# Kernel optimization log

Measured on AMD Instinct MI355X. Metric: run time of the kernel, lower is better.

The kernel has to match this reference:

```python
import jax, jax.numpy as jnp
import numpy as np

D = 1024      # embedding_size
H = 16        # num_heads
HD = D // H   # head_size
EPS = 1e-5


def setup_inputs() -> dict:
    key = jax.random.key(0)
    ks = jax.random.split(key, 12)
    s_in = 1.0 / np.sqrt(D)
    s_hid = 1.0 / np.sqrt(4 * D)
    return {
        "x": jax.random.normal(ks[0], (2, 2048, D), dtype=jnp.float32),
        # per-head projections, no bias: [H, D, HD]
        "Wq": jax.random.normal(ks[1], (H, D, HD), dtype=jnp.float32) * s_in,
        "Wk": jax.random.normal(ks[2], (H, D, HD), dtype=jnp.float32) * s_in,
        "Wv": jax.random.normal(ks[3], (H, D, HD), dtype=jnp.float32) * s_in,
        "Wo": jax.random.normal(ks[4], (D, D), dtype=jnp.float32) * s_in,
        "bo": jnp.zeros((D,), dtype=jnp.float32),
        "W1": jax.random.normal(ks[5], (D, 4 * D), dtype=jnp.float32) * s_in,
        "b1": jnp.zeros((4 * D,), dtype=jnp.float32),
        "W2": jax.random.normal(ks[6], (4 * D, D), dtype=jnp.float32) * s_hid,
        "b2": jnp.zeros((D,), dtype=jnp.float32),
        "g1": jnp.ones((D,), dtype=jnp.float32),
        "be1": jnp.zeros((D,), dtype=jnp.float32),
        "g2": jnp.ones((D,), dtype=jnp.float32),
        "be2": jnp.zeros((D,), dtype=jnp.float32),
    }


def _layernorm(x, g, b):
    mu = jnp.mean(x, axis=-1, keepdims=True)
    var = jnp.mean(jnp.square(x - mu), axis=-1, keepdims=True)
    return (x - mu) * jax.lax.rsqrt(var + EPS) * g + b


def _block(x, Wq, Wk, Wv, Wo, bo, W1, b1, W2, b2, g1, be1, g2, be2):
    B, T, _ = x.shape
    h = _layernorm(x, g1, be1)
    # per-head projections: [B, H, T, HD]
    q = jnp.einsum('btd,hde->bhte', h, Wq)
    k = jnp.einsum('btd,hde->bhte', h, Wk)
    v = jnp.einsum('btd,hde->bhte', h, Wv)
    # NOTE: original scales by embedding_size**-0.5 (x.shape[-1]), not head_size
    scores = jnp.einsum('bhte,bhse->bhts', q, k) * (D ** -0.5)
    mask = jnp.tril(jnp.ones((T, T), dtype=bool))
    scores = jnp.where(mask, scores, -jnp.inf)
    attn = jax.nn.softmax(scores, axis=-1)           # dropout = identity (eval)
    out = jnp.einsum('bhts,bhse->bhte', attn, v)      # [B, H, T, HD]
    out = out.transpose(0, 2, 1, 3).reshape(B, T, D)  # concat heads
    x = x + (out @ Wo + bo)
    h2 = _layernorm(x, g2, be2)
    ffn = jax.nn.relu(h2 @ W1 + b1) @ W2 + b2
    return x + ffn


def reference(x, Wq, Wk, Wv, Wo, bo, W1, b1, W2, b2, g1, be1, g2, be2):
    return _block(x, Wq, Wk, Wv, Wo, bo, W1, b1, W2, b2, g1, be1, g2, be2)
```

## Files before the change

### kernel.cpp

```cpp
#include <hip/hip_runtime.h>
#include <stdint.h>

typedef unsigned short u16;
typedef __attribute__((ext_vector_type(8))) __bf16 bf16x8;
typedef __attribute__((ext_vector_type(4))) float f32x4;

#define D_EMB 1024
#define NHEAD 16
#define HDIM 64
#define TSEQ 2048
#define NTOK 4096
#define NEG_BIG -1.0e30f

#define GLD16(lp, gp) __builtin_amdgcn_global_load_lds( \
    (const __attribute__((address_space(1))) unsigned int*)(gp), \
    (__attribute__((address_space(3))) unsigned int*)(lp), 16, 0, 0)

__device__ __forceinline__ float bf2f(u16 u) {
    union { unsigned int i; float f; } c; c.i = ((unsigned int)u) << 16; return c.f;
}
__device__ __forceinline__ u16 f2bf(float f) {
    union { float f; unsigned int i; } c; c.f = f;
    unsigned int r = (c.i + 0x7FFFu + ((c.i >> 16) & 1u)) >> 16;
    return (u16)r;
}
__device__ __forceinline__ void cp16(u16* dst, const u16* src) {
    *reinterpret_cast<uint4*>(dst) = *reinterpret_cast<const uint4*>(src);
}
__device__ __forceinline__ float load_in(const u16* p, size_t idx, int f32) {
    return f32 ? reinterpret_cast<const float*>(p)[idx] : bf2f(p[idx]);
}
__device__ __forceinline__ size_t tidx(int row, int col, int KB) {
    int c = (col & 7) | ((((col >> 3) ^ row) & 3) << 3);
    return ((size_t)((row >> 7) * KB + (col >> 5)) * 128 + (row & 127)) * 32 + c;
}

__global__ void detect_kernel(const u16* __restrict__ x, u16* __restrict__ fl) {
    if (threadIdx.x == 0) {
        int f = 0;
        for (int i = 0; i < 128; ++i) {
            float v = fabsf(bf2f(x[i]));
            if (!(v <= 1.0e3f)) f = 1;
        }
        fl[0] = (u16)f;
    }
}

__global__ __launch_bounds__(256) void transpose_tiled_kernel(
        const u16* __restrict__ X, u16* __restrict__ Xt, int KB,
        const u16* __restrict__ fl) {
    __shared__ __align__(16) u16 Ts[64 * 72];
    int f32 = fl[0];
    int bi = blockIdx.y, bj = blockIdx.x;
    int NS = gridDim.x * 64;
    int t = threadIdx.x;
    for (int p = 0; p < 2; ++p) {
        int idx = p * 256 + t;
        int row = idx >> 3, col8 = (idx & 7) * 8;
        size_t src = (size_t)(bi * 64 + row) * NS + bj * 64 + col8;
        if (f32) {
            for (int jj = 0; jj < 8; ++jj)
                Ts[row * 72 + col8 + jj] = f2bf(reinterpret_cast<const float*>(X)[src + jj]);
        } else {
            cp16(&Ts[row * 72 + col8], &X[src]);
        }
    }
    __syncthreads();
    for (int p = 0; p < 2; ++p) {
        int idx = p * 256 + t;
        int row = idx >> 3, col8 = (idx & 7) * 8;
        union { u16 u[8]; uint4 v; } tmp;
        for (int jj = 0; jj < 8; ++jj) tmp.u[jj] = Ts[(col8 + jj) * 72 + row];
        int n = bj * 64 + row, k0 = bi * 64 + col8;
        *reinterpret_cast<uint4*>(&Xt[tidx(n, k0, KB)]) = tmp.v;
    }
}

__global__ __launch_bounds__(256) void pack_qkv_kernel(
        const u16* __restrict__ Wq, const u16* __restrict__ Wk,
        const u16* __restrict__ Wv, u16* __restrict__ Wt,
        const u16* __restrict__ fl) {
    int f32 = fl[0];
    int idx = blockIdx.x * 256 + threadIdx.x;
    int e = idx & 63, d = (idx >> 6) & 1023, hh = (idx >> 16) & 15, sel = idx >> 20;
    const u16* W = (sel == 0) ? Wq : ((sel == 1) ? Wk : Wv);
    size_t src = (size_t)hh * (D_EMB * HDIM) + (size_t)d * HDIM + e;
    float v = f32 ? reinterpret_cast<const float*>(W)[src] : bf2f(W[src]);
    int n = sel * 1024 + hh * 64 + e;
    Wt[tidx(n, d, 32)] = f2bf(v);
}

__global__ __launch_bounds__(256) void ln_kernel(
        const u16* __restrict__ X, const u16* __restrict__ g,
        const u16* __restrict__ be, u16* __restrict__ Ht,
        const u16* __restrict__ fl) {
    int f32 = fl[0];
    int row = blockIdx.x;
    int t = threadIdx.x;
    float v[4];
    float s = 0.f, sq = 0.f;
    for (int i = 0; i < 4; ++i) {
        v[i] = load_in(X, (size_t)row * D_EMB + t + i * 256, f32);
        s += v[i]; sq += v[i] * v[i];
    }
    for (int m = 32; m; m >>= 1) { s += __shfl_down(s, m); sq += __shfl_down(sq, m); }
    __shared__ float red[8];
    int wid = t >> 6, lane = t & 63;
    if (lane == 0) { red[wid] = s; red[wid + 4] = sq; }
    __syncthreads();
    if (t == 0) {
        float S = red[0] + red[1] + red[2] + red[3];
        float SQ = red[4] + red[5] + red[6] + red[7];
        float mean = S * (1.f / 1024.f);
        float var = SQ * (1.f / 1024.f) - mean * mean;
        red[0] = mean; red[1] = rsqrtf(var + 1e-5f);
    }
    __syncthreads();
    float mean = red[0], rstd = red[1];
    for (int i = 0; i < 4; ++i) {
        int c = t + i * 256;
        float hv = (v[i] - mean) * rstd * load_in(g, c, f32) + load_in(be, c, f32);
        Ht[tidx(row, c, 32)] = f2bf(hv);
    }
}

template<int TAG, int TN>
__global__ __launch_bounds__(256) void gemm_t(
        const u16* __restrict__ At, const u16* __restrict__ Bt, u16* __restrict__ C,
        u16* __restrict__ C2,
        const u16* __restrict__ bias, const u16* __restrict__ res,
        int N, int K, int flags, int row_off,
        const u16* __restrict__ fl) {
    constexpr int NF = (TN == 128) ? 4 : 2;
    __shared__ __align__(16) u16 As2[2][4096];
    __shared__ __align__(16) u16 Bs2[2][TN * 32];
    int f32 = fl[0];
    int t = threadIdx.x;
    int gx = gridDim.x, gy = gridDim.y;
    int id = blockIdx.y * gx + blockIdx.x;
    int total = gx * gy;
    int xcd = id & 7, seq = id >> 3, P = total >> 3;
    int tpb = (P >= 32) ? 32 : 16;
    int th  = (P >= 32) ? 8 : 4;
    int tile = xcd * (P / tpb) + seq / tpb;
    int within = seq % tpb;
    int tiles_x = gx >> 2;
    int bx = (tile % tiles_x) * 4 + (within & 3);
    int by = (tile / tiles_x) * th + (within >> 2);
    int n0 = bx * TN, m0 = by * 128;
    int w = t >> 6, lane = t & 63, quad = lane >> 4, l16 = lane & 15;
    int wm = (TN == 128) ? (w >> 1) * 64 : (w & 1) * 64;
    int wn = (TN == 128) ? (w & 1) * 64  : (w >> 1) * 32;
    int KB = K >> 5;
    int kb0 = (seq * (KB >> 5)) & (KB - 1);
    const u16* Ab = At + (size_t)(m0 >> 7) * KB * 4096 + w * 512 + lane * 8;
    const u16* Bb = Bt + (size_t)(n0 >> 7) * KB * 4096
                       + ((TN == 64) ? (n0 & 64) * 32 : 0) + w * 512 + lane * 8;

    auto stage = [&](int buf, int kb) {
        const u16* ga = Ab + (size_t)kb * 4096;
        const u16* gb = Bb + (size_t)kb * 4096;
        u16* la = &As2[buf][w * 512];
        u16* lb = &Bs2[buf][w * 512];
        GLD16(la, ga);
        GLD16(la + 2048, ga + 2048);
        GLD16(lb, gb);
        if constexpr (TN == 128) { GLD16(lb + 2048, gb + 2048); }
    };

    const f32x4 fz = {0.f, 0.f, 0.f, 0.f};
    f32x4 acc[4][NF];
    for (int mt = 0; mt < 4; ++mt)
        for (int nt = 0; nt < NF; ++nt) acc[mt][nt] = fz;

    stage(0, kb0);
    __syncthreads();
    int kb = kb0;
    for (int it = 0; it < KB; ++it) {
        int cur = it & 1;
        int kn = (kb + 1 == KB) ? 0 : kb + 1;
        if (it + 1 < KB) stage(cur ^ 1, kn);
        bf16x8 af[4], bfr[NF];
        for (int mt = 0; mt < 4; ++mt) {
            int r = wm + mt * 16 + l16;
            af[mt] = *reinterpret_cast<const bf16x8*>(
                &As2[cur][r * 32 + (((quad ^ r) & 3) << 3)]);
        }
        for (int nt = 0; nt < NF; ++nt) {
            int r = wn + nt * 16 + l16;
            bfr[nt] = *reinterpret_cast<const bf16x8*>(
                &Bs2[cur][r * 32 + (((quad ^ r) & 3) << 3)]);
        }
        for (int mt = 0; mt < 4; ++mt)
            for (int nt = 0; nt < NF; ++nt)
                acc[mt][nt] = __builtin_amdgcn_mfma_f32_16x16x32_bf16(af[mt], bfr[nt], acc[mt][nt], 0, 0, 0);
        __syncthreads();
        kb = kn;
    }

    int relu_f = flags & 1, out_ext = flags & 2, c_tiled = flags & 4, qkvsp = flags & 8;
    if (qkvsp) {
        for (int mt = 0; mt < 4; ++mt)
            for (int nt = 0; nt < NF; ++nt) {
                int gc = n0 + wn + nt * 16 + l16;
                int grb = m0 + wm + mt * 16 + quad * 4;
                if (gc < 2048) {
                    for (int r = 0; r < 4; ++r)
                        C[(size_t)(grb + r) * 2048 + gc] = f2bf(acc[mt][nt][r]);
                } else {
                    int hh = (gc - 2048) >> 6, d = gc & 63;
                    int bb = grb >> 11, s = grb & 2047;
                    union { u16 u[4]; uint2 v; } pk;
                    for (int r = 0; r < 4; ++r) pk.u[r] = f2bf(acc[mt][nt][r]);
                    *reinterpret_cast<uint2*>(
                        &C2[(((size_t)bb * 16 + hh) * 64 + d) * 2048 + s]) = pk.v;
                }
            }
        return;
    }
    for (int mt = 0; mt < 4; ++mt)
        for (int nt = 0; nt < NF; ++nt)
            for (int r = 0; r < 4; ++r) {
                int gr = m0 + wm + mt * 16 + quad * 4 + r;
                int gc = n0 + wn + nt * 16 + l16;
                float v = acc[mt][nt][r];
                if (bias) v += load_in(bias, gc, f32);
                if (relu_f) v = v > 0.f ? v : 0.f;
                size_t oidx = (size_t)(row_off + gr) * N + gc;
                if (res) v += load_in(res, oidx, f32);
                if (c_tiled)      C[tidx(gr, gc, N >> 5)] = f2bf(v);
                else if (out_ext && f32) reinterpret_cast<float*>(C)[oidx] = v;
                else              C[oidx] = f2bf(v);
            }
}

template<int TAG, int KBL, int TN>
__global__ __launch_bounds__(256) void gemm_sk_t(
        const u16* __restrict__ At, const u16* __restrict__ Bt,
        float* __restrict__ Pp, int N, int K) {
    constexpr int NF = (TN == 128) ? 4 : 2;
    __shared__ __align__(16) u16 As2[2][4096];
    __shared__ __align__(16) u16 Bs2[2][TN * 32];
    int t = threadIdx.x;
    int gx = gridDim.x, gy = gridDim.y;
    int id = blockIdx.y * gx + blockIdx.x;
    int total = gx * gy;
    int xcd = id & 7, seq = id >> 3, P = total >> 3;
    int tpb = (P >= 32) ? 32 : 16;
    int th  = (P >= 32) ? 8 : 4;
    int tile = xcd * (P / tpb) + seq / tpb;
    int within = seq % tpb;
    int tiles_x = gx >> 2;
    int bx = (tile % tiles_x) * 4 + (within & 3);
    int by = (tile / tiles_x) * th + (within >> 2);
    int n0 = bx * TN, m0 = by * 128;
    int w = t >> 6, lane = t & 63, quad = lane >> 4, l16 = lane & 15;
    int wm = (TN == 128) ? (w >> 1) * 64 : (w & 1) * 64;
    int wn = (TN == 128) ? (w & 1) * 64  : (w >> 1) * 32;
    int KB = K >> 5;
    int kstart = blockIdx.z * KBL;
    int rel0 = seq & (KBL - 1);
    const u16* Ab = At + (size_t)(m0 >> 7) * KB * 4096 + w * 512 + lane * 8;
    const u16* Bb = Bt + (size_t)(n0 >> 7) * KB * 4096
                       + ((TN == 64) ? (n0 & 64) * 32 : 0) + w * 512 + lane * 8;

    auto stage = [&](int buf, int kb) {
        const u16* ga = Ab + (size_t)kb * 4096;
        const u16* gb = Bb + (size_t)kb * 4096;
        u16* la = &As2[buf][w * 512];
        u16* lb = &Bs2[buf][w * 512];
        GLD16(la, ga);
        GLD16(la + 2048, ga + 2048);
        GLD16(lb, gb);
        if constexpr (TN == 128) { GLD16(lb + 2048, gb + 2048); }
    };

    const f32x4 fz = {0.f, 0.f, 0.f, 0.f};
    f32x4 acc[4][NF];
    for (int mt = 0; mt < 4; ++mt)
        for (int nt = 0; nt < NF; ++nt) acc[mt][nt] = fz;

    stage(0, kstart + rel0);
    __syncthreads();
    for (int it = 0; it < KBL; ++it) {
        int cur = it & 1;
        if (it + 1 < KBL)
            stage(cur ^ 1, kstart + ((rel0 + it + 1) & (KBL - 1)));
        bf16x8 af[4], bfr[NF];
        for (int mt = 0; mt < 4; ++mt) {
            int r = wm + mt * 16 + l16;
            af[mt] = *reinterpret_cast<const bf16x8*>(
                &As2[cur][r * 32 + (((quad ^ r) & 3) << 3)]);
        }
        for (int nt = 0; nt < NF; ++nt) {
            int r = wn + nt * 16 + l16;
            bfr[nt] = *reinterpret_cast<const bf16x8*>(
                &Bs2[cur][r * 32 + (((quad ^ r) & 3) << 3)]);
        }
        for (int mt = 0; mt < 4; ++mt)
            for (int nt = 0; nt < NF; ++nt)
                acc[mt][nt] = __builtin_amdgcn_mfma_f32_16x16x32_bf16(af[mt], bfr[nt], acc[mt][nt], 0, 0, 0);
        __syncthreads();
    }

    for (int mt = 0; mt < 4; ++mt)
        for (int nt = 0; nt < NF; ++nt)
            for (int r = 0; r < 4; ++r) {
                int gr = m0 + wm + mt * 16 + quad * 4 + r;
                int gc = n0 + wn + nt * 16 + l16;
                atomicAdd(&Pp[(size_t)gr * N + gc], acc[mt][nt][r]);
            }
}

__global__ __launch_bounds__(256) void zero_f32_kernel(float* __restrict__ p) {
    const f32x4 fz = {0.f, 0.f, 0.f, 0.f};
    reinterpret_cast<f32x4*>(p)[(size_t)blockIdx.x * 256 + threadIdx.x] = fz;
}

__global__ __launch_bounds__(256) void ffn_fin_kernel(
        const float* __restrict__ Pp, const u16* __restrict__ b2,
        u16* __restrict__ out, int row_off, const u16* __restrict__ fl) {
    int f32 = fl[0];
    size_t i = ((size_t)blockIdx.x * 256 + threadIdx.x) * 4;
    int col = (int)(i & 1023);
    f32x4 pv = *reinterpret_cast<const f32x4*>(Pp + i);
    size_t o = (size_t)row_off * 1024 + i;
    if (f32) {
        float* of = reinterpret_cast<float*>(out);
        f32x4 ov = *reinterpret_cast<f32x4*>(of + o);
        for (int j = 0; j < 4; ++j)
            ov[j] += pv[j] + load_in(b2, col + j, 1);
        *reinterpret_cast<f32x4*>(of + o) = ov;
    } else {
        for (int j = 0; j < 4; ++j) {
            float v = bf2f(out[o + j]) + pv[j] + bf2f(b2[col + j]);
            out[o + j] = f2bf(v);
        }
    }
}

__global__ __launch_bounds__(256) void oproj_fin_kernel(
        const float* __restrict__ Pp, const u16* __restrict__ bo,
        const u16* __restrict__ x, u16* __restrict__ out,
        const u16* __restrict__ fl) {
    int f32 = fl[0];
    size_t i = ((size_t)blockIdx.x * 256 + threadIdx.x) * 4;
    int col = (int)(i & 1023);
    f32x4 pv = *reinterpret_cast<const f32x4*>(Pp + i);
    if (f32) {
        const float* xf = reinterpret_cast<const float*>(x);
        float* of = reinterpret_cast<float*>(out);
        f32x4 ov;
        for (int j = 0; j < 4; ++j)
            ov[j] = xf[i + j] + pv[j] + load_in(bo, col + j, 1);
        *reinterpret_cast<f32x4*>(of + i) = ov;
    } else {
        for (int j = 0; j < 4; ++j) {
            float v = bf2f(x[i + j]) + pv[j] + bf2f(bo[col + j]);
            out[i + j] = f2bf(v);
        }
    }
}

__global__ __launch_bounds__(128) void flash_kernel(
        const u16* __restrict__ qk, const u16* __restrict__ vt,
        u16* __restrict__ attn_t) {
    __shared__ __align__(16) u16 Ps[32 * 72];
    int t = threadIdx.x;
    int px = blockIdx.x & 15, rh = blockIdx.x >> 4;
    int b = blockIdx.y >> 4, h = blockIdx.y & 15;
    int wid = t >> 6, lane = t & 63, quad = lane >> 4, l16 = lane & 15;
    int g = rh * 2 + wid;
    const size_t seq_base = (size_t)b * TSEQ;
    const u16* vplane = vt + (size_t)(b * 16 + h) * 64 * 2048;

    for (int half = 0; half < 2; ++half) {
        int tq = half ? px : (31 - px);

        bf16x8 aq[2];
        for (int kit = 0; kit < 2; ++kit)
            aq[kit] = *reinterpret_cast<const bf16x8*>(
                &qk[(seq_base + tq * 64 + g * 16 + l16) * 2048 + h * 64 + kit * 32 + quad * 8]);

        const f32x4 fz = {0.f, 0.f, 0.f, 0.f};
        float m_run[4], l_run[4];
        f32x4 o[4];
        for (int r = 0; r < 4; ++r) { m_run[r] = NEG_BIG; l_run[r] = 0.f; }
        for (int nt = 0; nt < 4; ++nt) o[nt] = fz;

        for (int j = 0; j <= tq; ++j) {
            f32x4 sa[4];
            for (int nt = 0; nt < 4; ++nt) sa[nt] = fz;
            for (int kit = 0; kit < 2; ++kit) {
                for (int nt = 0; nt < 4; ++nt) {
                    bf16x8 bk = *reinterpret_cast<const bf16x8*>(
                        &qk[(seq_base + j * 64 + nt * 16 + l16) * 2048 + 1024 + h * 64 + kit * 32 + quad * 8]);
                    sa[nt] = __builtin_amdgcn_mfma_f32_16x16x32_bf16(aq[kit], bk, sa[nt], 0, 0, 0);
                }
            }

            float p_val[4][4];
            int qbase = tq * 64 + g * 16 + quad * 4;
            int sbase = j * 64 + l16;
            for (int r = 0; r < 4; ++r) {
                float sv[4];
                float mx = NEG_BIG;
                for (int nt = 0; nt < 4; ++nt) {
                    float xv = sa[nt][r] * 0.03125f;
                    if (sbase + nt * 16 > qbase + r) xv = NEG_BIG;
                    sv[nt] = xv;
                    mx = fmaxf(mx, xv);
                }
                for (int m = 1; m < 16; m <<= 1) mx = fmaxf(mx, __shfl_xor(mx, m));
                float mnew = fmaxf(m_run[r], mx);
                float alpha = __expf(m_run[r] - mnew);
                m_run[r] = mnew;
                float rs = 0.f;
                for (int nt = 0; nt < 4; ++nt) {
                    float pv = __expf(sv[nt] - mnew);
                    p_val[nt][r] = pv;
                    rs += pv;
                }
                for (int m = 1; m < 16; m <<= 1) rs += __shfl_xor(rs, m);
                l_run[r] = l_run[r] * alpha + rs;
                for (int nt = 0; nt < 4; ++nt) o[nt][r] *= alpha;
            }

            for (int nt = 0; nt < 4; ++nt)
                for (int r = 0; r < 4; ++r)
                    Ps[(wid * 16 + quad * 4 + r) * 72 + nt * 16 + l16] = f2bf(p_val[nt][r]);

            for (int kit = 0; kit < 2; ++kit) {
                bf16x8 ap = *reinterpret_cast<const bf16x8*>(
                    &Ps[(wid * 16 + l16) * 72 + kit * 32 + quad * 8]);
                for (int nt = 0; nt < 4; ++nt) {
                    bf16x8 bv = *reinterpret_cast<const bf16x8*>(
                        &vplane[(size_t)(nt * 16 + l16) * 2048 + j * 64 + kit * 32 + quad * 8]);
                    o[nt] = __builtin_amdgcn_mfma_f32_16x16x32_bf16(ap, bv, o[nt], 0, 0, 0);
                }
            }
        }

        for (int nt = 0; nt < 4; ++nt)
            for (int r = 0; r < 4; ++r) {
                int trow = (int)seq_base + tq * 64 + g * 16 + quad * 4 + r;
                int col = h * 64 + nt * 16 + l16;
                attn_t[tidx(trow, col, 32)] = f2bf(o[nt][r] / l_run[r]);
            }
    }
}

extern "C" void kernel_launch(void* const* d_in, const int* in_sizes, int n_in,
                              void* d_out, int out_size, void* d_ws, size_t ws_size,
                              hipStream_t stream) {
    const u16* x   = (const u16*)d_in[0];
    const u16* Wq  = (const u16*)d_in[1];
    const u16* Wk  = (const u16*)d_in[2];
    const u16* Wv  = (const u16*)d_in[3];
    const u16* Wo  = (const u16*)d_in[4];
    const u16* bo  = (const u16*)d_in[5];
    const u16* W1  = (const u16*)d_in[6];
    const u16* b1  = (const u16*)d_in[7];
    const u16* W2  = (const u16*)d_in[8];
    const u16* b2  = (const u16*)d_in[9];
    const u16* g1  = (const u16*)d_in[10];
    const u16* be1 = (const u16*)d_in[11];
    const u16* g2  = (const u16*)d_in[12];
    const u16* be2 = (const u16*)d_in[13];
    u16* out = (u16*)d_out;

    const size_t M1 = (size_t)1 << 20;
    u16* ws    = (u16*)d_ws;
    u16* qk    = ws;
    u16* vt    = ws + 8 * M1;
    u16* W2t   = ws;
    u16* a1    = ws + 4 * M1;
    u16* h     = ws + 12 * M1;
    u16* attn  = ws + 12 * M1;
    u16* h2    = ws + 12 * M1;
    u16* Wtq   = ws + 16 * M1;
    u16* Wot   = ws + 16 * M1;
    u16* W1t   = ws + 16 * M1;
    u16* fl    = ws + 20 * M1;
    float* Pp  = reinterpret_cast<float*>(ws + 21 * M1);
    bool sk = ws_size >= ((size_t)58 << 20);

    detect_kernel<<<1, 64, 0, stream>>>(x, fl);

    pack_qkv_kernel<<<(3 * 16 * 1024 * 64) / 256, 256, 0, stream>>>(Wq, Wk, Wv, Wtq, fl);
    ln_kernel<<<NTOK, 256, 0, stream>>>(x, g1, be1, h, fl);
    gemm_t<0, 64><<<dim3(48, 32), 256, 0, stream>>>(
        h, Wtq, qk, vt, nullptr, nullptr, 3072, 1024, 8, 0, fl);

    transpose_tiled_kernel<<<dim3(16, 16), 256, 0, stream>>>(Wo, Wot, 32, fl);

    flash_kernel<<<dim3(32, 32), 128, 0, stream>>>(qk, vt, attn);

    if (sk) {
        zero_f32_kernel<<<4096, 256, 0, stream>>>(Pp);
        gemm_sk_t<2, 8, 64><<<dim3(16, 32, 4), 256, 0, stream>>>(attn, Wot, Pp, 1024, 1024);
        oproj_fin_kernel<<<4096, 256, 0, stream>>>(Pp, bo, x, out, fl);
    } else {
        gemm_t<1, 128><<<dim3(8, 32), 256, 0, stream>>>(
            attn, Wot, out, nullptr, bo, x, 1024, 1024, 2, 0, fl);
    }

    transpose_tiled_kernel<<<dim3(16, 64), 256, 0, stream>>>(W2, W2t, 128, fl);
    transpose_tiled_kernel<<<dim3(64, 16), 256, 0, stream>>>(W1, W1t, 32, fl);
    ln_kernel<<<NTOK, 256, 0, stream>>>(out, g2, be2, h2, fl);

    gemm_t<2, 64><<<dim3(64, 16), 256, 0, stream>>>(
        h2, W1t, a1, nullptr, b1, nullptr, 4096, 1024, 1 | 4, 0, fl);
    if (sk) {
        zero_f32_kernel<<<2048, 256, 0, stream>>>(Pp);
        gemm_sk_t<0, 32, 64><<<dim3(16, 16, 4), 256, 0, stream>>>(a1, W2t, Pp, 1024, 4096);
        ffn_fin_kernel<<<2048, 256, 0, stream>>>(Pp, b2, out, 0, fl);
    } else {
        gemm_t<4, 128><<<dim3(8, 16), 256, 0, stream>>>(
            a1, W2t, out, nullptr, b2, out, 1024, 4096, 2, 0, fl);
    }
    gemm_t<3, 64><<<dim3(64, 16), 256, 0, stream>>>(
        h2 + (size_t)2 * M1, W1t, a1, nullptr, b1, nullptr, 4096, 1024, 1 | 4, 0, fl);
    if (sk) {
        zero_f32_kernel<<<2048, 256, 0, stream>>>(Pp);
        gemm_sk_t<1, 32, 64><<<dim3(16, 16, 4), 256, 0, stream>>>(a1, W2t, Pp, 1024, 4096);
        ffn_fin_kernel<<<2048, 256, 0, stream>>>(Pp, b2, out, 2048, fl);
    } else {
        gemm_t<5, 128><<<dim3(8, 16), 256, 0, stream>>>(
            a1, W2t, out, nullptr, b2, out, 1024, 4096, 2, 2048, fl);
    }
}
```

Measured before the change: 626.9 us.

## Split long causal row across two waves with LDS softmax merge, skip masking on full tiles

The flash attention kernel now gives each 16-row group its own block, doubling the grid. Within a block, wave 0 handles the first 16 key tiles of the long row (31-px). Wave 1 handles the short row px and then the rest of the long row, and the two partial softmax states are merged through shared memory. Causal masking is applied only on diagonal tiles. The goal is to balance work between waves and raise parallelism, at the cost of one extra LDS merge and a barrier per block.

```diff
diff --git a/kernel.cpp b/kernel.cpp
--- a/kernel.cpp
+++ b/kernel.cpp
@@ -366,87 +366,118 @@
         const u16* __restrict__ qk, const u16* __restrict__ vt,
         u16* __restrict__ attn_t) {
     __shared__ __align__(16) u16 Ps[32 * 72];
+    __shared__ float Om[16 * 64];
+    __shared__ float MLm[32];
     int t = threadIdx.x;
-    int px = blockIdx.x & 15, rh = blockIdx.x >> 4;
+    int px = blockIdx.x & 15, g = blockIdx.x >> 4;
     int b = blockIdx.y >> 4, h = blockIdx.y & 15;
     int wid = t >> 6, lane = t & 63, quad = lane >> 4, l16 = lane & 15;
-    int g = rh * 2 + wid;
     const size_t seq_base = (size_t)b * TSEQ;
     const u16* vplane = vt + (size_t)(b * 16 + h) * 64 * 2048;
-
-    for (int half = 0; half < 2; ++half) {
-        int tq = half ? px : (31 - px);
-
-        bf16x8 aq[2];
+    int H = 31 - px;
+    const f32x4 fz = {0.f, 0.f, 0.f, 0.f};
+
+    bf16x8 aq[2];
+    float m_run[4], l_run[4];
+    f32x4 o[4];
+
+    auto load_q = [&](int tq) {
         for (int kit = 0; kit < 2; ++kit)
             aq[kit] = *reinterpret_cast<const bf16x8*>(
                 &qk[(seq_base + tq * 64 + g * 16 + l16) * 2048 + h * 64 + kit * 32 + quad * 8]);
-
-        const f32x4 fz = {0.f, 0.f, 0.f, 0.f};
-        float m_run[4], l_run[4];
-        f32x4 o[4];
+    };
+    auto reset = [&]() {
         for (int r = 0; r < 4; ++r) { m_run[r] = NEG_BIG; l_run[r] = 0.f; }
         for (int nt = 0; nt < 4; ++nt) o[nt] = fz;
-
-        for (int j = 0; j <= tq; ++j) {
-            f32x4 sa[4];
-            for (int nt = 0; nt < 4; ++nt) sa[nt] = fz;
-            for (int kit = 0; kit < 2; ++kit) {
-                for (int nt = 0; nt < 4; ++nt) {
-                    bf16x8 bk = *reinterpret_cast<const bf16x8*>(
-                        &qk[(seq_base + j * 64 + nt * 16 + l16) * 2048 + 1024 + h * 64 + kit * 32 + quad * 8]);
-                    sa[nt] = __builtin_amdgcn_mfma_f32_16x16x32_bf16(aq[kit], bk, sa[nt], 0, 0, 0);
-                }
-            }
-
-            float p_val[4][4];
-            int qbase = tq * 64 + g * 16 + quad * 4;
-            int sbase = j * 64 + l16;
-            for (int r = 0; r < 4; ++r) {
-                float sv[4];
-                float mx = NEG_BIG;
-                for (int nt = 0; nt < 4; ++nt) {
-                    float xv = sa[nt][r] * 0.03125f;
-                    if (sbase + nt * 16 > qbase + r) xv = NEG_BIG;
-                    sv[nt] = xv;
-                    mx = fmaxf(mx, xv);
-                }
-                for (int m = 1; m < 16; m <<= 1) mx = fmaxf(mx, __shfl_xor(mx, m));
-                float mnew = fmaxf(m_run[r], mx);
-                float alpha = __expf(m_run[r] - mnew);
-                m_run[r] = mnew;
-                float rs = 0.f;
-                for (int nt = 0; nt < 4; ++nt) {
-                    float pv = __expf(sv[nt] - mnew);
-                    p_val[nt][r] = pv;
-                    rs += pv;
-                }
-                for (int m = 1; m < 16; m <<= 1) rs += __shfl_xor(rs, m);
-                l_run[r] = l_run[r] * alpha + rs;
-                for (int nt = 0; nt < 4; ++nt) o[nt][r] *= alpha;
-            }
-
-            for (int nt = 0; nt < 4; ++nt)
-                for (int r = 0; r < 4; ++r)
-                    Ps[(wid * 16 + quad * 4 + r) * 72 + nt * 16 + l16] = f2bf(p_val[nt][r]);
-
-            for (int kit = 0; kit < 2; ++kit) {
-                bf16x8 ap = *reinterpret_cast<const bf16x8*>(
-                    &Ps[(wid * 16 + l16) * 72 + kit * 32 + quad * 8]);
-                for (int nt = 0; nt < 4; ++nt) {
-                    bf16x8 bv = *reinterpret_cast<const bf16x8*>(
-                        &vplane[(size_t)(nt * 16 + l16) * 2048 + j * 64 + kit * 32 + quad * 8]);
-                    o[nt] = __builtin_amdgcn_mfma_f32_16x16x32_bf16(ap, bv, o[nt], 0, 0, 0);
-                }
-            }
-        }
-
+    };
+    auto tile = [&](int tq, int j, int domask) {
+        f32x4 sa[4];
+        for (int nt = 0; nt < 4; ++nt) sa[nt] = fz;
+        for (int kit = 0; kit < 2; ++kit)
+            for (int nt = 0; nt < 4; ++nt) {
+                bf16x8 bk = *reinterpret_cast<const bf16x8*>(
+                    &qk[(seq_base + j * 64 + nt * 16 + l16) * 2048 + 1024 + h * 64 + kit * 32 + quad * 8]);
+                sa[nt] = __builtin_amdgcn_mfma_f32_16x16x32_bf16(aq[kit], bk, sa[nt], 0, 0, 0);
+            }
+        int qbase = tq * 64 + g * 16 + quad * 4;
+        int sbase = j * 64 + l16;
+        float p_val[4][4];
+        for (int r = 0; r < 4; ++r) {
+            float sv[4];
+            float mx = NEG_BIG;
+            for (int nt = 0; nt < 4; ++nt) {
+                float xv = sa[nt][r] * 0.03125f;
+                if (domask && (sbase + nt * 16 > qbase + r)) xv = NEG_BIG;
+                sv[nt] = xv;
+                mx = fmaxf(mx, xv);
+            }
+            for (int m = 1; m < 16; m <<= 1) mx = fmaxf(mx, __shfl_xor(mx, m));
+            float mnew = fmaxf(m_run[r], mx);
+            float alpha = __expf(m_run[r] - mnew);
+            m_run[r] = mnew;
+            float rs = 0.f;
+            for (int nt = 0; nt < 4; ++nt) {
+                float pv = __expf(sv[nt] - mnew);
+                p_val[nt][r] = pv;
+                rs += pv;
+            }
+            for (int m = 1; m < 16; m <<= 1) rs += __shfl_xor(rs, m);
+            l_run[r] = l_run[r] * alpha + rs;
+            for (int nt = 0; nt < 4; ++nt) o[nt][r] *= alpha;
+        }
+        for (int nt = 0; nt < 4; ++nt)
+            for (int r = 0; r < 4; ++r)
+                Ps[(wid * 16 + quad * 4 + r) * 72 + nt * 16 + l16] = f2bf(p_val[nt][r]);
+        for (int kit = 0; kit < 2; ++kit) {
+            bf16x8 ap = *reinterpret_cast<const bf16x8*>(
+                &Ps[(wid * 16 + l16) * 72 + kit * 32 + quad * 8]);
+            for (int nt = 0; nt < 4; ++nt) {
+                bf16x8 bv = *reinterpret_cast<const bf16x8*>(
+                    &vplane[(size_t)(nt * 16 + l16) * 2048 + j * 64 + kit * 32 + quad * 8]);
+                o[nt] = __builtin_amdgcn_mfma_f32_16x16x32_bf16(ap, bv, o[nt], 0, 0, 0);
+            }
+        }
+    };
+
+    if (wid == 0) {
+        load_q(H);
+        reset();
+        for (int j = 0; j < 16; ++j) tile(H, j, 0);
+    } else {
+        load_q(px);
+        reset();
+        for (int j = 0; j < px; ++j) tile(px, j, 0);
+        tile(px, px, 1);
         for (int nt = 0; nt < 4; ++nt)
             for (int r = 0; r < 4; ++r) {
-                int trow = (int)seq_base + tq * 64 + g * 16 + quad * 4 + r;
-                int col = h * 64 + nt * 16 + l16;
-                attn_t[tidx(trow, col, 32)] = f2bf(o[nt][r] / l_run[r]);
-            }
+                int trow = (int)seq_base + px * 64 + g * 16 + quad * 4 + r;
+                attn_t[tidx(trow, h * 64 + nt * 16 + l16, 32)] = f2bf(o[nt][r] / l_run[r]);
+            }
+        load_q(H);
+        reset();
+        for (int j = 16; j < H; ++j) tile(H, j, 0);
+        tile(H, H, 1);
+        for (int r = 0; r < 4; ++r) {
+            int row = quad * 4 + r;
+            if (l16 == 0) { MLm[row] = m_run[r]; MLm[16 + row] = l_run[r]; }
+            for (int nt = 0; nt < 4; ++nt)
+                Om[row * 64 + nt * 16 + l16] = o[nt][r];
+        }
+    }
+    __syncthreads();
+    if (wid == 0) {
+        for (int r = 0; r < 4; ++r) {
+            int row = quad * 4 + r;
+            float m1 = MLm[row], l1 = MLm[16 + row];
+            float mm = fmaxf(m_run[r], m1);
+            float a0 = __expf(m_run[r] - mm), a1 = __expf(m1 - mm);
+            float li = 1.f / (a0 * l_run[r] + a1 * l1);
+            int trow = (int)seq_base + H * 64 + g * 16 + row;
+            for (int nt = 0; nt < 4; ++nt) {
+                float val = (a0 * o[nt][r] + a1 * Om[row * 64 + nt * 16 + l16]) * li;
+                attn_t[tidx(trow, h * 64 + nt * 16 + l16, 32)] = f2bf(val);
+            }
+        }
     }
 }
 
@@ -494,7 +525,7 @@
 
     transpose_tiled_kernel<<<dim3(16, 16), 256, 0, stream>>>(Wo, Wot, 32, fl);
 
-    flash_kernel<<<dim3(32, 32), 128, 0, stream>>>(qk, vt, attn);
+    flash_kernel<<<dim3(64, 32), 128, 0, stream>>>(qk, vt, attn);
 
     if (sk) {
         zero_f32_kernel<<<4096, 256, 0, stream>>>(Pp);
```

After: 644.0 us. 2.7% more time.

## Fuse LN2 into o-proj epilogue, unsplit FFN, vectorize QKV weight pack

Applied to the files above, without the earlier changes.

The o-projection finalize kernel now also computes LayerNorm2 per row and writes the tiled h2 directly, which removes a separate ln_kernel pass over the residual. In the split-K path, the two half-batch FFN passes are merged into one full-token W1 GEMM and one W2 split-K GEMM, using a reorganized workspace layout. The QKV weight pack kernel now has each thread convert 8 consecutive d values and write one 16-byte store. In exchange it needs more workspace, and the LayerNorm variance uses E[x²]-mean², which is less numerically stable.

```diff
diff --git a/kernel.cpp b/kernel.cpp
--- a/kernel.cpp
+++ b/kernel.cpp
@@ -82,12 +82,17 @@
         const u16* __restrict__ fl) {
     int f32 = fl[0];
     int idx = blockIdx.x * 256 + threadIdx.x;
-    int e = idx & 63, d = (idx >> 6) & 1023, hh = (idx >> 16) & 15, sel = idx >> 20;
+    int e = idx & 63, d8 = (idx >> 6) & 127, hh = (idx >> 13) & 15, sel = idx >> 17;
     const u16* W = (sel == 0) ? Wq : ((sel == 1) ? Wk : Wv);
-    size_t src = (size_t)hh * (D_EMB * HDIM) + (size_t)d * HDIM + e;
-    float v = f32 ? reinterpret_cast<const float*>(W)[src] : bf2f(W[src]);
     int n = sel * 1024 + hh * 64 + e;
-    Wt[tidx(n, d, 32)] = f2bf(v);
+    size_t src = (size_t)hh * (D_EMB * HDIM) + (size_t)(d8 * 8) * HDIM + e;
+    union { u16 u[8]; uint4 v; } tmp;
+    for (int dd = 0; dd < 8; ++dd) {
+        float v = f32 ? reinterpret_cast<const float*>(W)[src + (size_t)dd * HDIM]
+                      : bf2f(W[src + (size_t)dd * HDIM]);
+        tmp.u[dd] = f2bf(v);
+    }
+    *reinterpret_cast<uint4*>(&Wt[tidx(n, d8 * 8, 32)]) = tmp.v;
 }
 
 __global__ __launch_bounds__(256) void ln_kernel(
@@ -339,26 +344,48 @@
     }
 }
 
-__global__ __launch_bounds__(256) void oproj_fin_kernel(
+__global__ __launch_bounds__(256) void oproj_fin_ln2_kernel(
         const float* __restrict__ Pp, const u16* __restrict__ bo,
-        const u16* __restrict__ x, u16* __restrict__ out,
-        const u16* __restrict__ fl) {
+        const u16* __restrict__ x, const u16* __restrict__ g2,
+        const u16* __restrict__ be2, u16* __restrict__ out,
+        u16* __restrict__ h2t, const u16* __restrict__ fl) {
     int f32 = fl[0];
-    size_t i = ((size_t)blockIdx.x * 256 + threadIdx.x) * 4;
-    int col = (int)(i & 1023);
-    f32x4 pv = *reinterpret_cast<const f32x4*>(Pp + i);
+    int row = blockIdx.x;
+    int t = threadIdx.x;
+    size_t base = (size_t)row * 1024 + t * 4;
+    f32x4 pv = *reinterpret_cast<const f32x4*>(Pp + base);
+    float v[4];
+    float s = 0.f, sq = 0.f;
+    for (int j = 0; j < 4; ++j) {
+        v[j] = load_in(x, base + j, f32) + pv[j] + load_in(bo, t * 4 + j, f32);
+        s += v[j]; sq += v[j] * v[j];
+    }
     if (f32) {
-        const float* xf = reinterpret_cast<const float*>(x);
-        float* of = reinterpret_cast<float*>(out);
-        f32x4 ov;
-        for (int j = 0; j < 4; ++j)
-            ov[j] = xf[i + j] + pv[j] + load_in(bo, col + j, 1);
-        *reinterpret_cast<f32x4*>(of + i) = ov;
+        f32x4 ov = {v[0], v[1], v[2], v[3]};
+        *reinterpret_cast<f32x4*>(reinterpret_cast<float*>(out) + base) = ov;
     } else {
-        for (int j = 0; j < 4; ++j) {
-            float v = bf2f(x[i + j]) + pv[j] + bf2f(bo[col + j]);
-            out[i + j] = f2bf(v);
-        }
+        union { u16 u[4]; uint2 q; } pk;
+        for (int j = 0; j < 4; ++j) pk.u[j] = f2bf(v[j]);
+        *reinterpret_cast<uint2*>(&out[base]) = pk.q;
+    }
+    for (int m = 32; m; m >>= 1) { s += __shfl_down(s, m); sq += __shfl_down(sq, m); }
+    __shared__ float red[8];
+    int wid = t >> 6, lane = t & 63;
+    if (lane == 0) { red[wid] = s; red[wid + 4] = sq; }
+    __syncthreads();
+    if (t == 0) {
+        float S = red[0] + red[1] + red[2] + red[3];
+        float SQ = red[4] + red[5] + red[6] + red[7];
+        float mean = S * (1.f / 1024.f);
+        float var = SQ * (1.f / 1024.f) - mean * mean;
+        red[0] = mean; red[1] = rsqrtf(var + 1e-5f);
+    }
+    __syncthreads();
+    float mean = red[0], rstd = red[1];
+    for (int j = 0; j < 4; ++j) {
+        int c = t * 4 + j;
+        float hv = (v[j] - mean) * rstd * load_in(g2, c, f32) + load_in(be2, c, f32);
+        h2t[tidx(row, c, 32)] = f2bf(hv);
     }
 }
 
@@ -470,62 +497,78 @@
     u16* out = (u16*)d_out;
 
     const size_t M1 = (size_t)1 << 20;
-    u16* ws    = (u16*)d_ws;
-    u16* qk    = ws;
-    u16* vt    = ws + 8 * M1;
-    u16* W2t   = ws;
-    u16* a1    = ws + 4 * M1;
-    u16* h     = ws + 12 * M1;
-    u16* attn  = ws + 12 * M1;
-    u16* h2    = ws + 12 * M1;
-    u16* Wtq   = ws + 16 * M1;
-    u16* Wot   = ws + 16 * M1;
-    u16* W1t   = ws + 16 * M1;
-    u16* fl    = ws + 20 * M1;
-    float* Pp  = reinterpret_cast<float*>(ws + 21 * M1);
+    u16* ws = (u16*)d_ws;
     bool sk = ws_size >= ((size_t)58 << 20);
 
-    detect_kernel<<<1, 64, 0, stream>>>(x, fl);
-
-    pack_qkv_kernel<<<(3 * 16 * 1024 * 64) / 256, 256, 0, stream>>>(Wq, Wk, Wv, Wtq, fl);
-    ln_kernel<<<NTOK, 256, 0, stream>>>(x, g1, be1, h, fl);
-    gemm_t<0, 64><<<dim3(48, 32), 256, 0, stream>>>(
-        h, Wtq, qk, vt, nullptr, nullptr, 3072, 1024, 8, 0, fl);
-
-    transpose_tiled_kernel<<<dim3(16, 16), 256, 0, stream>>>(Wo, Wot, 32, fl);
-
-    flash_kernel<<<dim3(32, 32), 128, 0, stream>>>(qk, vt, attn);
-
     if (sk) {
-        zero_f32_kernel<<<4096, 256, 0, stream>>>(Pp);
-        gemm_sk_t<2, 8, 64><<<dim3(16, 32, 4), 256, 0, stream>>>(attn, Wot, Pp, 1024, 1024);
-        oproj_fin_kernel<<<4096, 256, 0, stream>>>(Pp, bo, x, out, fl);
+        u16* qk   = ws;
+        u16* vt   = ws + 8 * M1;
+        u16* attn = ws + 12 * M1;
+        u16* W1t  = ws + 16 * M1;
+        u16* h    = ws + 20 * M1;
+        u16* Wot  = ws + 20 * M1;
+        u16* h2   = ws + 20 * M1;
+        u16* Wtq  = ws + 24 * M1;
+        u16* W2t  = ws + 24 * M1;
+        u16* a1   = ws;
+        float* PpO = reinterpret_cast<float*>(ws);
+        float* PpF = reinterpret_cast<float*>(ws + 16 * M1);
+        u16* fl   = ws + 28 * M1;
+
+        detect_kernel<<<1, 64, 0, stream>>>(x, fl);
+
+        pack_qkv_kernel<<<1536, 256, 0, stream>>>(Wq, Wk, Wv, Wtq, fl);
+        ln_kernel<<<NTOK, 256, 0, stream>>>(x, g1, be1, h, fl);
+        gemm_t<0, 64><<<dim3(48, 32), 256, 0, stream>>>(
+            h, Wtq, qk, vt, nullptr, nullptr, 3072, 1024, 8, 0, fl);
+
+        transpose_tiled_kernel<<<dim3(16, 16), 256, 0, stream>>>(Wo, Wot, 32, fl);
+
+        flash_kernel<<<dim3(32, 32), 128, 0, stream>>>(qk, vt, attn);
+
+        zero_f32_kernel<<<4096, 256, 0, stream>>>(PpO);
+        gemm_sk_t<2, 8, 64><<<dim3(16, 32, 4), 256, 0, stream>>>(attn, Wot, PpO, 1024, 1024);
+        oproj_fin_ln2_kernel<<<4096, 256, 0, stream>>>(PpO, bo, x, g2, be2, out, h2, fl);
+
+        transpose_tiled_kernel<<<dim3(16, 64), 256, 0, stream>>>(W2, W2t, 128, fl);
+        transpose_tiled_kernel<<<dim3(64, 16), 256, 0, stream>>>(W1, W1t, 32, fl);
+
+        gemm_t<2, 64><<<dim3(64, 32), 256, 0, stream>>>(
+            h2, W1t, a1, nullptr, b1, nullptr, 4096, 1024, 1 | 4, 0, fl);
+        zero_f32_kernel<<<4096, 256, 0, stream>>>(PpF);
+        gemm_sk_t<0, 32, 64><<<dim3(16, 32, 4), 256, 0, stream>>>(a1, W2t, PpF, 1024, 4096);
+        ffn_fin_kernel<<<4096, 256, 0, stream>>>(PpF, b2, out, 0, fl);
     } else {
+        u16* qk   = ws;
+        u16* vt   = ws + 8 * M1;
+        u16* h    = ws + 12 * M1;
+        u16* attn = ws + 12 * M1;
+        u16* h2   = ws + 12 * M1;
+        u16* Wtq  = ws + 16 * M1;
+        u16* Wot  = ws + 16 * M1;
+        u16* W1t  = ws + 16 * M1;
+        u16* W2t  = ws;
+        u16* a1   = ws + 4 * M1;
+        u16* fl   = ws + 20 * M1;
+
+        detect_kernel<<<1, 64, 0, stream>>>(x, fl);
+        pack_qkv_kernel<<<1536, 256, 0, stream>>>(Wq, Wk, Wv, Wtq, fl);
+        ln_kernel<<<NTOK, 256, 0, stream>>>(x, g1, be1, h, fl);
+        gemm_t<0, 64><<<dim3(48, 32), 256, 0, stream>>>(
+            h, Wtq, qk, vt, nullptr, nullptr, 3072, 1024, 8, 0, fl);
+        transpose_tiled_kernel<<<dim3(16, 16), 256, 0, stream>>>(Wo, Wot, 32, fl);
+        flash_kernel<<<dim3(32, 32), 128, 0, stream>>>(qk, vt, attn);
         gemm_t<1, 128><<<dim3(8, 32), 256, 0, stream>>>(
             attn, Wot, out, nullptr, bo, x, 1024, 1024, 2, 0, fl);
-    }
-
-    transpose_tiled_kernel<<<dim3(16, 64), 256, 0, stream>>>(W2, W2t, 128, fl);
-    transpose_tiled_kernel<<<dim3(64, 16), 256, 0, stream>>>(W1, W1t, 32, fl);
-    ln_kernel<<<NTOK, 256, 0, stream>>>(out, g2, be2, h2, fl);
-
-    gemm_t<2, 64><<<dim3(64, 16), 256, 0, stream>>>(
-        h2, W1t, a1, nullptr, b1, nullptr, 4096, 1024, 1 | 4, 0, fl);
-    if (sk) {
-        zero_f32_kernel<<<2048, 256, 0, stream>>>(Pp);
-        gemm_sk_t<0, 32, 64><<<dim3(16, 16, 4), 256, 0, stream>>>(a1, W2t, Pp, 1024, 4096);
-        ffn_fin_kernel<<<2048, 256, 0, stream>>>(Pp, b2, out, 0, fl);
-    } else {
+        transpose_tiled_kernel<<<dim3(16, 64), 256, 0, stream>>>(W2, W2t, 128, fl);
+        transpose_tiled_kernel<<<dim3(64, 16), 256, 0, stream>>>(W1, W1t, 32, fl);
+        ln_kernel<<<NTOK, 256, 0, stream>>>(out, g2, be2, h2, fl);
+        gemm_t<2, 64><<<dim3(64, 16), 256, 0, stream>>>(
+            h2, W1t, a1, nullptr, b1, nullptr, 4096, 1024, 1 | 4, 0, fl);
         gemm_t<4, 128><<<dim3(8, 16), 256, 0, stream>>>(
             a1, W2t, out, nullptr, b2, out, 1024, 4096, 2, 0, fl);
-    }
-    gemm_t<3, 64><<<dim3(64, 16), 256, 0, stream>>>(
-        h2 + (size_t)2 * M1, W1t, a1, nullptr, b1, nullptr, 4096, 1024, 1 | 4, 0, fl);
-    if (sk) {
-        zero_f32_kernel<<<2048, 256, 0, stream>>>(Pp);
-        gemm_sk_t<1, 32, 64><<<dim3(16, 16, 4), 256, 0, stream>>>(a1, W2t, Pp, 1024, 4096);
-        ffn_fin_kernel<<<2048, 256, 0, stream>>>(Pp, b2, out, 2048, fl);
-    } else {
+        gemm_t<3, 64><<<dim3(64, 16), 256, 0, stream>>>(
+            h2 + (size_t)2 * M1, W1t, a1, nullptr, b1, nullptr, 4096, 1024, 1 | 4, 0, fl);
         gemm_t<5, 128><<<dim3(8, 16), 256, 0, stream>>>(
             a1, W2t, out, nullptr, b2, out, 1024, 4096, 2, 2048, fl);
     }
```

Result: faster. 614.3 us (-2.0%).
